# Performance work log

Measured on AMD Instinct MI355X. Metric: run time of the kernel, lower is better.

## Reference

```python
import jax, jax.numpy as jnp
import numpy as np

DIM = 768
NUM_HEADS = 12
HEAD_DIM = DIM // NUM_HEADS
SCALE = HEAD_DIM ** -0.5


def setup_inputs() -> dict:
    key = jax.random.key(0)
    ks = jax.random.split(key, 9)
    B, L, C = 4, 1024, DIM
    x = jax.random.normal(ks[0], (B, L, C), jnp.float32)
    q_ape = jax.random.normal(ks[1], (1, L, C), jnp.float32)
    k_ape = jax.random.normal(ks[2], (1, L, C), jnp.float32)
    attn_pos = jax.random.normal(ks[3], (1, NUM_HEADS, L, L), jnp.float32)
    s = C ** -0.5
    # torch Linear weights: (out_features, in_features)
    Wq = jax.random.normal(ks[4], (C, C), jnp.float32) * s
    Wk = jax.random.normal(ks[5], (C, C), jnp.float32) * s
    Wv = jax.random.normal(ks[6], (C, C), jnp.float32) * s
    Wp = jax.random.normal(ks[7], (C, C), jnp.float32) * s
    bp = jax.random.normal(ks[8], (C,), jnp.float32) * 0.01
    return {"x": x, "q_ape": q_ape, "k_ape": k_ape, "attn_pos": attn_pos,
            "Wq": Wq, "Wk": Wk, "Wv": Wv, "Wp": Wp, "bp": bp}


def _split_heads(t):
    # (B, L, C) -> (B, H, L, D)
    B, L, C = t.shape
    return t.reshape(B, L, NUM_HEADS, HEAD_DIM).transpose(0, 2, 1, 3)


def reference(x, q_ape, k_ape, attn_pos, Wq, Wk, Wv, Wp, bp):
    B, L, C = x.shape
    q = _split_heads((x + q_ape) @ Wq.T)          # (B,H,L,D)
    k = _split_heads((x + k_ape) @ Wk.T)          # (B,H,L,D)
    v = _split_heads(x @ Wv.T)                    # (B,H,L,D)
    attn = jnp.einsum('bhqd,bhkd->bhqk', q, k) * SCALE + attn_pos
    attn = jax.nn.softmax(attn, axis=-1)
    out = jnp.einsum('bhqk,bhkd->bhqd', attn, v)  # (B,H,L,D)
    out = out.transpose(0, 2, 1, 3).reshape(B, L, C)
    return out @ Wp.T + bp
```

## Files before the change

kernel.cpp:

```cpp
#include <hip/hip_runtime.h>
#include <stdint.h>

#define NH 12
#define HD 64
#define NB 4
#define SEQ 1024
#define CDIM 768
#define MTOT (NB*SEQ)
#define MC   (MTOT*CDIM)
#define LC   (SEQ*CDIM)
#define WSZ  (CDIM*CDIM)
#define LST  104
#define EST  136
#define L2E  1.44269504f
#define BHSZ (SEQ*HD)

typedef __attribute__((ext_vector_type(4))) float f32x4;
typedef __attribute__((ext_vector_type(8))) __bf16 bf16x8;
typedef __attribute__((ext_vector_type(8))) short short8;
typedef __attribute__((ext_vector_type(4))) unsigned short ushort4v;
typedef unsigned short u16;

static __device__ __forceinline__ f32x4 mfma16(short8 a, short8 b, f32x4 c) {
  return __builtin_amdgcn_mfma_f32_16x16x32_bf16(
      __builtin_bit_cast(bf16x8, a), __builtin_bit_cast(bf16x8, b), c, 0, 0, 0);
}
static __device__ __forceinline__ u16 f2bf(float f) {
  unsigned u = __float_as_uint(f);
  u += 0x7FFFu + ((u >> 16) & 1u);
  return (u16)(u >> 16);
}
static __device__ __forceinline__ float bf2f(u16 h) {
  return __uint_as_float(((unsigned)h) << 16);
}
static __device__ __forceinline__ void lds_load16(const void* g, void* l) {
  __builtin_amdgcn_global_load_lds(
      (const __attribute__((address_space(1))) void*)g,
      (__attribute__((address_space(3))) void*)l, 16, 0, 0);
}

#define PREP_BLKS (MC / 4 / 256)
#define CONV_N4   ((4 * WSZ + CDIM) / 4)
#define CONV_BLKS ((CONV_N4 + 255) / 256)
__global__ __launch_bounds__(256) void prep_all(
    const float* __restrict__ xp, const float* __restrict__ qp,
    const float* __restrict__ kp, const float* __restrict__ Wq,
    const float* __restrict__ Wk, const float* __restrict__ Wv,
    const float* __restrict__ Wp, const float* __restrict__ bp,
    u16* __restrict__ Xq, u16* __restrict__ Xk, u16* __restrict__ Xv,
    u16* __restrict__ Wb) {
  int bid = blockIdx.x;
  if (bid < PREP_BLKS) {
    int i4 = bid * 256 + threadIdx.x;
    int a4 = i4 % (LC / 4);
    f32x4 xx = ((const f32x4*)xp)[i4];
    f32x4 qq = ((const f32x4*)qp)[a4];
    f32x4 kk = ((const f32x4*)kp)[a4];
    ushort4v oq, ok, ov;
#pragma unroll
    for (int j = 0; j < 4; j++) {
      oq[j] = f2bf(xx[j] + qq[j]);
      ok[j] = f2bf(xx[j] + kk[j]);
      ov[j] = f2bf(xx[j]);
    }
    ((ushort4v*)Xq)[i4] = oq;
    ((ushort4v*)Xk)[i4] = ok;
    ((ushort4v*)Xv)[i4] = ov;
  } else {
    int i4 = (bid - PREP_BLKS) * 256 + threadIdx.x;
    if (i4 >= CONV_N4) return;
    int sel = i4 / (WSZ / 4);
    int off = i4 - sel * (WSZ / 4);
    const float* src = sel == 0 ? Wq : sel == 1 ? Wk : sel == 2 ? Wv
                     : sel == 3 ? Wp : bp;
    f32x4 v = ((const f32x4*)src)[off];
    ushort4v o;
#pragma unroll
    for (int j = 0; j < 4; j++) o[j] = f2bf(v[j]);
    ((ushort4v*)Wb)[i4] = o;
  }
}

static __device__ __forceinline__ void gemm_core(
    const u16* __restrict__ Ab, const u16* __restrict__ Wb,
    short* As, short* Bs, f32x4 acc[4][4]) {
  const int t = threadIdx.x;
  const int lane = t & 63, w = t >> 6, quad = lane >> 4, l16 = lane & 15;
  const int wm = (w >> 1) * 64, wn = (w & 1) * 64;
  const int row4 = t >> 2, chunk = (t & 3) * 8;
  for (int k0 = 0; k0 < CDIM; k0 += 64) {
#pragma unroll
    for (int hh = 0; hh < 2; hh++) {
      const u16* ga = Ab + row4 * CDIM + k0 + hh * 32 + chunk;
      const u16* gb = Wb + row4 * CDIM + k0 + hh * 32 + chunk;
      lds_load16(ga,             (char*)As + hh * 8192 + t * 16);
      lds_load16(ga + 64 * CDIM, (char*)As + hh * 8192 + 4096 + t * 16);
      lds_load16(gb,             (char*)Bs + hh * 8192 + t * 16);
      lds_load16(gb + 64 * CDIM, (char*)Bs + hh * 8192 + 4096 + t * 16);
    }
    __syncthreads();
#pragma unroll
    for (int hh = 0; hh < 2; hh++) {
      const short* Ah = As + hh * 4096;
      const short* Bh = Bs + hh * 4096;
      short8 af[4], bw[4];
#pragma unroll
      for (int i = 0; i < 4; i++)
        af[i] = *(const short8*)(Ah + (wm + i * 16 + l16) * 32 + quad * 8);
#pragma unroll
      for (int j = 0; j < 4; j++)
        bw[j] = *(const short8*)(Bh + (wn + j * 16 + l16) * 32 + quad * 8);
#pragma unroll
      for (int i = 0; i < 4; i++)
#pragma unroll
        for (int j = 0; j < 4; j++)
          acc[i][j] = mfma16(af[i], bw[j], acc[i][j]);
    }
    __syncthreads();
  }
}

__global__ __launch_bounds__(256) void gemm_qkv(
    const u16* __restrict__ Xq, const u16* __restrict__ Xk, const u16* __restrict__ Xv,
    const u16* __restrict__ Wq, const u16* __restrict__ Wk, const u16* __restrict__ Wv,
    u16* __restrict__ Q, u16* __restrict__ K, u16* __restrict__ Vt) {
  __shared__ __align__(16) short S[128 * EST];
  short* As = S;
  short* Bs = S + 8192;
  const int z = blockIdx.z;
  const int m0 = blockIdx.y * 128, n0 = blockIdx.x * 128;
  const u16* A = (z == 0 ? Xq : z == 1 ? Xk : Xv) + m0 * CDIM;
  const u16* W = (z == 0 ? Wq : z == 1 ? Wk : Wv) + n0 * CDIM;
  f32x4 acc[4][4];
#pragma unroll
  for (int i = 0; i < 4; i++)
#pragma unroll
    for (int j = 0; j < 4; j++) acc[i][j] = 0.f;
  gemm_core(A, W, As, Bs, acc);

  const int t = threadIdx.x, lane = t & 63, w = t >> 6;
  const int quad = lane >> 4, l16 = lane & 15;
  const int wm = (w >> 1) * 64, wn = (w & 1) * 64;
  const float qs = (z == 0) ? 0.125f : 1.0f;

#pragma unroll
  for (int i = 0; i < 4; i++)
#pragma unroll
    for (int j = 0; j < 4; j++)
#pragma unroll
      for (int r = 0; r < 4; r++) {
        int mr = wm + i * 16 + quad * 4 + r;
        int nc = wn + j * 16 + l16;
        if (z < 2) S[mr * EST + nc] = (short)f2bf(acc[i][j][r] * qs);
        else       S[nc * EST + mr] = (short)f2bf(acc[i][j][r]);
      }
  __syncthreads();

  const int row = t >> 3, ch = t & 7;
  const int b = m0 >> 10, lbase = m0 & 1023;
  if (z == 0) {
#pragma unroll
    for (int cp = 0; cp < 2; cp++) {
      int h = (n0 >> 6) + cp;
#pragma unroll
      for (int rp = 0; rp < 4; rp++) {
        int mr = row + rp * 32;
        short8 v = *(const short8*)(S + mr * EST + cp * 64 + ch * 8);
        *(short8*)(Q + ((((size_t)(b * NH + h)) << 10) + lbase + mr) * HD + ch * 8) = v;
      }
    }
  } else if (z == 1) {
#pragma unroll
    for (int cp = 0; cp < 2; cp++) {
      int h = (n0 >> 6) + cp;
      u16* Kp = K + (size_t)(b * NH + h) * BHSZ;
#pragma unroll
      for (int rp = 0; rp < 4; rp++) {
        int mr = row + rp * 32;
        int tok = lbase + mr;
        short8 v = *(const short8*)(S + mr * EST + cp * 64 + ch * 8);
        *(short8*)(Kp + (((tok >> 4) * 8 + ch) * 16 + (tok & 15)) * 8) = v;
      }
    }
  } else {
#pragma unroll
    for (int rp = 0; rp < 4; rp++) {
      int rn = row + rp * 32;
      int h = (n0 + rn) >> 6, d = rn & 63;
      u16* Vp = Vt + (size_t)(b * NH + h) * BHSZ;
      int jv = d >> 4, ld16 = d & 15;
#pragma unroll
      for (int cp = 0; cp < 2; cp++) {
        int tok = lbase + cp * 64 + ch * 8;
        short8 v = *(const short8*)(S + rn * EST + cp * 64 + ch * 8);
        *(short8*)(Vp + ((((tok >> 6) * 4 + jv) * 8 + ((tok >> 3) & 7)) * 16 + ld16) * 8) = v;
      }
    }
  }
}

__global__ __launch_bounds__(256, 3) void attn(
    const u16* __restrict__ Q, const u16* __restrict__ Kf, const u16* __restrict__ Vf,
    const float* __restrict__ pos, u16* __restrict__ O) {
  __shared__ __align__(16) short Ps[4 * 16 * LST];
  const int t = threadIdx.x, lane = t & 63, w = t >> 6;
  const int quad = lane >> 4, l16 = lane & 15;

  const int lid = blockIdx.x;
  const int k8 = lid & 7, m = lid >> 3;
  const int g = k8 * 24 + (m >> 2), b = m & 3;
  const int h = g >> 4, qt = g & 15;
  const int bh = b * NH + h;
  const int q0 = qt * 64 + w * 16;

  const u16* Kg = Kf + (size_t)bh * BHSZ;
  const u16* Vg = Vf + (size_t)bh * BHSZ;
  const float* Pg = pos + (size_t)(h * SEQ + q0) * SEQ;
  short* Pw = Ps + w * 16 * LST;
  const int fo = quad * 128 + l16 * 8;

  const u16* Qg = Q + ((size_t)bh * SEQ + q0) * HD;
  const short8 qa0 = *(const short8*)(Qg + l16 * HD + quad * 8);
  const short8 qa1 = *(const short8*)(Qg + l16 * HD + 32 + quad * 8);

  f32x4 o[4];
  float lrow[4];
#pragma unroll
  for (int j = 0; j < 4; j++) o[j] = 0.f;
#pragma unroll
  for (int r = 0; r < 4; r++) lrow[r] = 0.f;

  short8 kb0[4], kb1[4];
  float pf[16];
#pragma unroll
  for (int j = 0; j < 4; j++) {
    kb0[j] = *(const short8*)(Kg + j * 1024 + fo);
    kb1[j] = *(const short8*)(Kg + j * 1024 + 512 + fo);
  }
#pragma unroll
  for (int j = 0; j < 4; j++)
#pragma unroll
    for (int r = 0; r < 4; r++)
      pf[j * 4 + r] = Pg[(quad * 4 + r) * SEQ + j * 16 + l16] * L2E;

#pragma unroll 1
  for (int kt = 0; kt < 16; ++kt) {
    const int kbase = kt * 4096;
    short8 vb0[4], vb1[4];
#pragma unroll
    for (int j = 0; j < 4; j++) {
      vb0[j] = *(const short8*)(Vg + kbase + j * 1024 + fo);
      vb1[j] = *(const short8*)(Vg + kbase + j * 1024 + 512 + fo);
    }
    f32x4 s[4];
#pragma unroll
    for (int j = 0; j < 4; j++) {
      f32x4 zz = 0.f;
      s[j] = mfma16(qa1, kb1[j], mfma16(qa0, kb0[j], zz));
    }
#pragma unroll
    for (int j = 0; j < 4; j++)
#pragma unroll
      for (int r = 0; r < 4; r++) {
        float e = __builtin_amdgcn_exp2f(fmaf(s[j][r], L2E, pf[j * 4 + r]));
        unsigned bits = __float_as_uint(e);
        Pw[(quad * 4 + r) * LST + j * 16 + l16] = (short)(bits >> 16);
        lrow[r] += __uint_as_float(bits & 0xFFFF0000u);
      }
    if (kt < 15) {
      const int nb = kbase + 4096;
#pragma unroll
      for (int j = 0; j < 4; j++) {
        kb0[j] = *(const short8*)(Kg + nb + j * 1024 + fo);
        kb1[j] = *(const short8*)(Kg + nb + j * 1024 + 512 + fo);
      }
      const float* pg = Pg + (kt + 1) * 64;
#pragma unroll
      for (int j = 0; j < 4; j++)
#pragma unroll
        for (int r = 0; r < 4; r++)
          pf[j * 4 + r] = pg[(quad * 4 + r) * SEQ + j * 16 + l16] * L2E;
    }
    const short8 pa0 = *(const short8*)(Pw + l16 * LST + quad * 8);
    const short8 pa1 = *(const short8*)(Pw + l16 * LST + 32 + quad * 8);
#pragma unroll
    for (int j = 0; j < 4; j++)
      o[j] = mfma16(pa1, vb1[j], mfma16(pa0, vb0[j], o[j]));
  }

#pragma unroll
  for (int off = 1; off < 16; off <<= 1)
#pragma unroll
    for (int r = 0; r < 4; r++) lrow[r] += __shfl_xor(lrow[r], off);

  u16* Og = O + ((size_t)b * SEQ + q0) * CDIM + h * HD;
  float inv[4];
#pragma unroll
  for (int r = 0; r < 4; r++) inv[r] = 1.0f / lrow[r];
#pragma unroll
  for (int j = 0; j < 4; j++)
#pragma unroll
    for (int r = 0; r < 4; r++)
      Og[(quad * 4 + r) * CDIM + j * 16 + l16] = f2bf(o[j][r] * inv[r]);
}

__global__ __launch_bounds__(256) void gemm_proj(
    const u16* __restrict__ Oin, const u16* __restrict__ Wp,
    const u16* __restrict__ bp, float* __restrict__ out) {
  __shared__ __align__(16) short As[8192], Bs[8192];
  const int m0 = blockIdx.y * 128, n0 = blockIdx.x * 128;
  f32x4 acc[4][4];
#pragma unroll
  for (int i = 0; i < 4; i++)
#pragma unroll
    for (int j = 0; j < 4; j++) acc[i][j] = 0.f;
  gemm_core(Oin + m0 * CDIM, Wp + n0 * CDIM, As, Bs, acc);

  const int t = threadIdx.x, lane = t & 63, w = t >> 6;
  const int quad = lane >> 4, l16 = lane & 15;
  const int wm = (w >> 1) * 64, wn = (w & 1) * 64;
#pragma unroll
  for (int i = 0; i < 4; i++) {
    int mrow = m0 + wm + i * 16 + quad * 4;
#pragma unroll
    for (int j = 0; j < 4; j++) {
      int n = n0 + wn + j * 16 + l16;
      float bias = bf2f(bp[n]);
#pragma unroll
      for (int r = 0; r < 4; r++)
        out[(mrow + r) * CDIM + n] = acc[i][j][r] + bias;
    }
  }
}

extern "C" void kernel_launch(void* const* d_in, const int* in_sizes, int n_in,
                              void* d_out, int out_size, void* d_ws, size_t ws_size,
                              hipStream_t stream) {
  (void)in_sizes; (void)n_in; (void)out_size;
  const size_t OFF_XQ = 0, OFF_XK = (size_t)MC, OFF_XV = 2ull * MC,
               OFF_Q = 3ull * MC, OFF_K = 4ull * MC, OFF_VT = 5ull * MC,
               OFF_W = 6ull * MC, TOT = OFF_W + 4ull * WSZ + 1024;
  const size_t NEED = 2 * TOT;
  if (ws_size < NEED) return;

  u16* ws = (u16*)d_ws;
  u16 *Xq = ws + OFF_XQ, *Xk = ws + OFF_XK, *Xv = ws + OFF_XV;
  u16 *Qb = ws + OFF_Q, *Kb = ws + OFF_K, *Vt = ws + OFF_VT;
  u16 *Wb = ws + OFF_W;
  u16 *Wqb = Wb, *Wkb = Wb + WSZ, *Wvb = Wb + 2ull * WSZ,
      *Wpb = Wb + 3ull * WSZ, *bpb = Wb + 4ull * WSZ;
  u16* Ob = Xq;

  prep_all<<<PREP_BLKS + CONV_BLKS, 256, 0, stream>>>(
      (const float*)d_in[0], (const float*)d_in[1], (const float*)d_in[2],
      (const float*)d_in[4], (const float*)d_in[5], (const float*)d_in[6],
      (const float*)d_in[7], (const float*)d_in[8], Xq, Xk, Xv, Wb);
  gemm_qkv<<<dim3(6, 32, 3), 256, 0, stream>>>(Xq, Xk, Xv, Wqb, Wkb, Wvb,
                                               Qb, Kb, Vt);
  attn<<<dim3(768), 256, 0, stream>>>(Qb, Kb, Vt, (const float*)d_in[3], Ob);
  gemm_proj<<<dim3(6, 32), 256, 0, stream>>>(Ob, Wpb, bpb, (float*)d_out);
}
```

Baseline: 218.2 us.

## Split attention key range across two wave halves and merge partials in LDS

The attention kernel grows to 512 threads per block. Each of the two 4-wave halves handles half of the key tiles for the same 16-row query slices, and the partial outputs and row sums are combined through shared memory before the final write. This raises parallelism and latency hiding within each block, since the grid of 768 blocks stays the same while each wave's serial loop is halved. In exchange it adds two block barriers, an LDS reduction step and more waves competing for registers. It relies on the kernel having no running-max rescaling, so partial sums can simply be added.

```diff
diff --git a/kernel.cpp b/kernel.cpp
--- a/kernel.cpp
+++ b/kernel.cpp
@@ -12,6 +12,7 @@
 #define WSZ  (CDIM*CDIM)
 #define LST  104
 #define EST  136
+#define CST  68
 #define L2E  1.44269504f
 #define BHSZ (SEQ*HD)
 
@@ -199,19 +200,20 @@
   }
 }
 
-__global__ __launch_bounds__(256, 3) void attn(
+__global__ __launch_bounds__(512, 6) void attn(
     const u16* __restrict__ Q, const u16* __restrict__ Kf, const u16* __restrict__ Vf,
     const float* __restrict__ pos, u16* __restrict__ O) {
-  __shared__ __align__(16) short Ps[4 * 16 * LST];
+  __shared__ __align__(16) short Ps[8 * 16 * LST];
   const int t = threadIdx.x, lane = t & 63, w = t >> 6;
   const int quad = lane >> 4, l16 = lane & 15;
+  const int wsub = w & 3, half = w >> 2;
 
   const int lid = blockIdx.x;
   const int k8 = lid & 7, m = lid >> 3;
   const int g = k8 * 24 + (m >> 2), b = m & 3;
   const int h = g >> 4, qt = g & 15;
   const int bh = b * NH + h;
-  const int q0 = qt * 64 + w * 16;
+  const int q0 = qt * 64 + wsub * 16;
 
   const u16* Kg = Kf + (size_t)bh * BHSZ;
   const u16* Vg = Vf + (size_t)bh * BHSZ;
@@ -230,22 +232,26 @@
 #pragma unroll
   for (int r = 0; r < 4; r++) lrow[r] = 0.f;
 
+  const int kt0 = half * 8;
   short8 kb0[4], kb1[4];
   float pf[16];
 #pragma unroll
   for (int j = 0; j < 4; j++) {
-    kb0[j] = *(const short8*)(Kg + j * 1024 + fo);
-    kb1[j] = *(const short8*)(Kg + j * 1024 + 512 + fo);
-  }
-#pragma unroll
-  for (int j = 0; j < 4; j++)
-#pragma unroll
-    for (int r = 0; r < 4; r++)
-      pf[j * 4 + r] = Pg[(quad * 4 + r) * SEQ + j * 16 + l16] * L2E;
+    kb0[j] = *(const short8*)(Kg + kt0 * 4096 + j * 1024 + fo);
+    kb1[j] = *(const short8*)(Kg + kt0 * 4096 + j * 1024 + 512 + fo);
+  }
+  {
+    const float* pg = Pg + kt0 * 64;
+#pragma unroll
+    for (int j = 0; j < 4; j++)
+#pragma unroll
+      for (int r = 0; r < 4; r++)
+        pf[j * 4 + r] = pg[(quad * 4 + r) * SEQ + j * 16 + l16] * L2E;
+  }
 
 #pragma unroll 1
-  for (int kt = 0; kt < 16; ++kt) {
-    const int kbase = kt * 4096;
+  for (int kk = 0; kk < 8; ++kk) {
+    const int kbase = (kt0 + kk) * 4096;
     short8 vb0[4], vb1[4];
 #pragma unroll
     for (int j = 0; j < 4; j++) {
@@ -267,14 +273,14 @@
         Pw[(quad * 4 + r) * LST + j * 16 + l16] = (short)(bits >> 16);
         lrow[r] += __uint_as_float(bits & 0xFFFF0000u);
       }
-    if (kt < 15) {
+    if (kk < 7) {
       const int nb = kbase + 4096;
 #pragma unroll
       for (int j = 0; j < 4; j++) {
         kb0[j] = *(const short8*)(Kg + nb + j * 1024 + fo);
         kb1[j] = *(const short8*)(Kg + nb + j * 1024 + 512 + fo);
       }
-      const float* pg = Pg + (kt + 1) * 64;
+      const float* pg = Pg + (kt0 + kk + 1) * 64;
 #pragma unroll
       for (int j = 0; j < 4; j++)
 #pragma unroll
@@ -292,6 +298,30 @@
   for (int off = 1; off < 16; off <<= 1)
 #pragma unroll
     for (int r = 0; r < 4; r++) lrow[r] += __shfl_xor(lrow[r], off);
+
+  __syncthreads();
+  float* Cb = (float*)Ps;
+  const int cb = wsub * (16 * CST + 16);
+  if (half) {
+#pragma unroll
+    for (int j = 0; j < 4; j++)
+#pragma unroll
+      for (int r = 0; r < 4; r++)
+        Cb[cb + (quad * 4 + r) * CST + j * 16 + l16] = o[j][r];
+    if (l16 == 0) {
+#pragma unroll
+      for (int r = 0; r < 4; r++) Cb[cb + 16 * CST + quad * 4 + r] = lrow[r];
+    }
+  }
+  __syncthreads();
+  if (half) return;
+#pragma unroll
+  for (int r = 0; r < 4; r++) lrow[r] += Cb[cb + 16 * CST + quad * 4 + r];
+#pragma unroll
+  for (int j = 0; j < 4; j++)
+#pragma unroll
+    for (int r = 0; r < 4; r++)
+      o[j][r] += Cb[cb + (quad * 4 + r) * CST + j * 16 + l16];
 
   u16* Og = O + ((size_t)b * SEQ + q0) * CDIM + h * HD;
   float inv[4];
@@ -357,6 +387,6 @@
       (const float*)d_in[7], (const float*)d_in[8], Xq, Xk, Xv, Wb);
   gemm_qkv<<<dim3(6, 32, 3), 256, 0, stream>>>(Xq, Xk, Xv, Wqb, Wkb, Wvb,
                                                Qb, Kb, Vt);
-  attn<<<dim3(768), 256, 0, stream>>>(Qb, Kb, Vt, (const float*)d_in[3], Ob);
+  attn<<<dim3(768), 512, 0, stream>>>(Qb, Kb, Vt, (const float*)d_in[3], Ob);
   gemm_proj<<<dim3(6, 32), 256, 0, stream>>>(Ob, Wpb, bpb, (float*)d_out);
 }
```

Measured after the change: 557.8 us. +155.6%, slower.
